# Optimization experiments

Hardware: AMD Instinct MI355X
Metric: run time of the kernel (lower is better)

## Reference

```python
import jax, jax.numpy as jnp
import numpy as np

R = 8
EPS = 1e-08
EPSS = 1e-12


def _diff_x(x, r):
    left = x[:, :, r:2 * r + 1]
    middle = x[:, :, 2 * r + 1:] - x[:, :, :-2 * r - 1]
    right = x[:, :, -1:] - x[:, :, -2 * r - 1:-r - 1]
    return jnp.concatenate([left, middle, right], axis=2)


def _diff_y(x, r):
    left = x[:, :, :, r:2 * r + 1]
    middle = x[:, :, :, 2 * r + 1:] - x[:, :, :, :-2 * r - 1]
    right = x[:, :, :, -1:] - x[:, :, :, -2 * r - 1:-r - 1]
    return jnp.concatenate([left, middle, right], axis=3)


def box_filter(x, r):
    # cumsum-based (2r+1)x(2r+1) box sum with clamped borders (matches torch BoxFilter)
    return _diff_y(jnp.cumsum(_diff_x(jnp.cumsum(x, axis=2), r), axis=3), r)


def bilinear_resize(x, H, W):
    # F.interpolate(mode='bilinear', align_corners=True) for NCHW
    n, c, h, w = x.shape
    ys = jnp.linspace(0.0, h - 1.0, H)
    xs = jnp.linspace(0.0, w - 1.0, W)
    y0 = jnp.floor(ys).astype(jnp.int32)
    x0 = jnp.floor(xs).astype(jnp.int32)
    y1 = jnp.minimum(y0 + 1, h - 1)
    x1 = jnp.minimum(x0 + 1, w - 1)
    wy = (ys - y0).astype(x.dtype)[None, None, :, None]
    wx = (xs - x0).astype(x.dtype)[None, None, None, :]
    rows = jnp.take(x, y0, axis=2) * (1.0 - wy) + jnp.take(x, y1, axis=2) * wy
    return jnp.take(rows, x0, axis=3) * (1.0 - wx) + jnp.take(rows, x1, axis=3) * wx


def setup_inputs() -> dict:
    key = jax.random.key(0)
    k1, k2, k3, k4 = jax.random.split(key, 4)
    return {
        "lr_x": jax.random.normal(k1, (4, 3, 256, 256), dtype=jnp.float32),
        "lr_y": jax.random.normal(k2, (4, 3, 256, 256), dtype=jnp.float32),
        "hr_x": jax.random.normal(k3, (4, 3, 1024, 1024), dtype=jnp.float32),
        "l_a": jax.random.uniform(k4, (4, 3, 256, 256), dtype=jnp.float32),
    }


def reference(lr_x, lr_y, hr_x, l_a):
    n, c, h, w = lr_x.shape
    _, _, hh, wh = hr_x.shape
    dt = lr_x.dtype

    N = box_filter(jnp.ones((1, 1, h, w), dtype=dt), R)  # local window counts

    l_a = jnp.abs(l_a) + EPSS
    l_t = l_a / jnp.sum(l_a)

    mean_a = box_filter(l_a) if False else box_filter(l_a, R) / N
    mean_a2xy = box_filter(l_a * l_a * lr_x * lr_y, R) / N
    mean_tax = box_filter(l_t * l_a * lr_x, R) / N
    mean_ay = box_filter(l_a * lr_y, R) / N
    mean_a2x2 = box_filter(l_a * l_a * lr_x * lr_x, R) / N
    mean_ax = box_filter(l_a * lr_x, R) / N

    temp = jnp.abs(mean_a2x2 - N * mean_tax * mean_ax)
    A = (mean_a2xy - N * mean_tax * mean_ay) / (temp + EPS)
    b = (mean_ay - A * mean_ax) / mean_a

    A = box_filter(A, R) / N
    b = box_filter(b, R) / N

    mean_A = bilinear_resize(A, hh, wh)
    mean_b = bilinear_resize(b, hh, wh)
    return (mean_A * hr_x + mean_b).astype(jnp.float32)
```

## Files before the change

### kernel.cpp

```cpp
#include <hip/hip_runtime.h>

#define RAD 8
#define HH 256
#define WW 256
#define NC 12
#define PS (HH*WW)

#define NA 52
#define NM 36
#define AP 53
#define CP 37

__device__ __forceinline__ int swz768(int b) { return (b & 7) * 96 + (b >> 3); }
__device__ __forceinline__ int swz576(int b) { return (b & 7) * 72 + (b >> 3); }

__device__ __forceinline__ float run17(float x) {
    float s = x + __shfl_up(x, 1, 64);
    s += __shfl_up(s, 2, 64);
    s += __shfl_up(s, 4, 64);
    s += __shfl_up(s, 8, 64);
    s += __shfl_up(x, 16, 64);
    return s;
}

__global__ __launch_bounds__(256) void k_reduce(const float* __restrict__ la,
                                                float* __restrict__ partials) {
    int tid = threadIdx.x;
    __shared__ float ls[4];
    const float4* p4 = (const float4*)la;
    int base = blockIdx.x * 2048 + tid;
    float s = 0.f;
    #pragma unroll
    for (int i = 0; i < 8; i++) {
        float4 v = p4[base + i * 256];
        s += (fabsf(v.x) + 1e-12f) + (fabsf(v.y) + 1e-12f) +
             (fabsf(v.z) + 1e-12f) + (fabsf(v.w) + 1e-12f);
    }
    for (int off = 32; off > 0; off >>= 1) s += __shfl_down(s, off, 64);
    int lane = tid & 63, wid = tid >> 6;
    if (lane == 0) ls[wid] = s;
    __syncthreads();
    if (tid == 0) partials[blockIdx.x] = ls[0] + ls[1] + ls[2] + ls[3];
}

__global__ __launch_bounds__(256) void k_ab(const float* __restrict__ la,
                                            const float* __restrict__ lx,
                                            const float* __restrict__ ly,
                                            const float* __restrict__ partials,
                                            float* __restrict__ Ab,
                                            float* __restrict__ Bb) {
    int tid = threadIdx.x, lane = tid & 63, wv = tid >> 6;
    int gw = swz576(blockIdx.x) * 4 + wv;
    int p  = gw / 192;
    int r  = gw - p * 192;
    int s  = r >> 5;
    int bd = r & 31;
    int i0 = bd << 3;
    int C0 = s * 48;
    int col = C0 - 8 + lane;
    bool vc = (col >= 0) && (col < WW);
    int colc = min(max(col, 0), WW - 1);
    const float* pa = la + p * PS + colc;
    const float* px = lx + p * PS + colc;
    const float* py = ly + p * PS + colc;

    float psum = partials[lane] + ((lane < 32) ? partials[lane + 64] : 0.0f);
    #pragma unroll
    for (int off = 32; off > 0; off >>= 1) psum += __shfl_xor(psum, off, 64);
    float invS = 1.0f / psum;

    int  cA  = C0 - 16 + lane;
    bool vcA = (lane >= 16) && (cA < WW);
    float cxA = (float)(min(cA + RAD, WW - 1) - max(cA - RAD, 0) + 1);

    float s0 = 0, s1 = 0, s2 = 0, s3 = 0, s4 = 0, s5 = 0;
    auto accum = [&](int rr, float sg) {
        float va = 0.f, vx = 0.f, vy = 0.f;
        if (vc) { int o = rr * WW; va = pa[o]; vx = px[o]; vy = py[o]; }
        float a  = vc ? (fabsf(va) + 1e-12f) : 0.f;
        float ax = a * vx, ay = a * vy;
        s0 = fmaf(sg, a, s0); s1 = fmaf(sg, ax, s1); s2 = fmaf(sg, ay, s2);
        s3 = fmaf(sg, a * ax, s3); s4 = fmaf(sg, ax * ax, s4); s5 = fmaf(sg, ax * ay, s5);
    };

    #pragma unroll
    for (int d = -8; d <= 8; ++d) {
        int rr = i0 + d;
        if (rr >= 0 && rr < HH) accum(rr, 1.0f);
    }

    float* Apl = Ab + p * PS;
    float* Bpl = Bb + p * PS;
    #pragma unroll
    for (int k = 0; k < 8; ++k) {
        int m = i0 + k;
        if (k > 0) {
            int ra = m + 8; if (ra < HH) accum(ra, 1.0f);
            int rs = m - 9; if (rs >= 0) accum(rs, -1.0f);
        }
        float h0 = run17(s0), h1 = run17(s1), h2 = run17(s2),
              h3 = run17(s3), h4 = run17(s4), h5 = run17(s5);
        float cy = (float)(min(m + RAD, HH - 1) - max(m - RAD, 0) + 1);
        float Nv = cxA * cy, invN = 1.0f / Nv;
        float m_a = h0 * invN, m_ax = h1 * invN, m_ay = h2 * invN;
        float m_tax = h3 * invN * invS;
        float m_a2x2 = h4 * invN, m_a2xy = h5 * invN;
        float tempv = fabsf(m_a2x2 - Nv * m_tax * m_ax);
        float Av = (m_a2xy - Nv * m_tax * m_ay) / (tempv + 1e-8f);
        float bv = (m_ay - Av * m_ax) / m_a;
        if (vcA) {
            int o = m * WW + cA;
            Apl[o] = Av;
            Bpl[o] = bv;
        }
    }
}

__global__ __launch_bounds__(256) void k_tile(const float* __restrict__ Ab,
                                              const float* __restrict__ Bb,
                                              const float* __restrict__ hrx,
                                              float* __restrict__ out) {
    __shared__ float sA[NA * AP], sB[NA * AP];
    __shared__ float sHA[NA * CP], sHB[NA * CP];
    float* mAb = sA;
    float* mBb = sB;

    int tid = threadIdx.x;
    int b  = swz768(blockIdx.x);
    int p  = b >> 6;
    int t  = b & 63;
    int ti = t >> 3, tj = t & 7;
    int I0 = ti << 7, J0 = tj << 7;
    int Lr0 = max(0, (I0 * 255) / 1023 - 1);
    int Lc0 = max(0, (J0 * 255) / 1023 - 1);

    const float* Apl = Ab + p * PS;
    const float* Bpl = Bb + p * PS;
    for (int idx = tid; idx < NA * NA; idx += 256) {
        int r = idx / NA, c = idx - r * NA;
        int gr = Lr0 - 8 + r, gc = Lc0 - 8 + c;
        float av = 0.f, bv = 0.f;
        if (gr >= 0 && gr < HH && gc >= 0 && gc < WW) {
            int o = gr * WW + gc;
            av = Apl[o]; bv = Bpl[o];
        }
        sA[r * AP + c] = av;
        sB[r * AP + c] = bv;
    }
    __syncthreads();

    for (int job = tid; job < 208; job += 256) {
        int row   = job % 52;
        int which = (job / 52) & 1;
        int strip = job / 104;
        const float* rp = (which ? sB : sA) + row * AP;
        float* dst = (which ? sHB : sHA) + row * CP;
        int c0 = strip * 18;
        float sum = 0.f;
        #pragma unroll
        for (int c = 0; c < 17; ++c) sum += rp[c0 + c];
        dst[c0] = sum;
        for (int jc = c0 + 1; jc < c0 + 18; ++jc) {
            sum += rp[jc + 16] - rp[jc - 1];
            dst[jc] = sum;
        }
    }
    __syncthreads();

    for (int job = tid; job < 144; job += 256) {
        int colc  = job % 36;
        int which = (job / 36) & 1;
        int strip = job / 72;
        const float* src = which ? sHB : sHA;
        float* dst = which ? mBb : mAb;
        int gjC = Lc0 + colc;
        float cxw = (float)(min(gjC + RAD, WW - 1) - max(gjC - RAD, 0) + 1);
        int r0 = strip * 18;
        float sum = 0.f;
        #pragma unroll
        for (int d = 0; d < 17; ++d) sum += src[(r0 + d) * CP + colc];
        for (int ic = r0; ic < r0 + 18; ++ic) {
            if (ic > r0) sum += src[(ic + 16) * CP + colc] - src[(ic - 1) * CP + colc];
            int giR = Lr0 + ic;
            float cyw = (float)(min(giR + RAD, HH - 1) - max(giR - RAD, 0) + 1);
            dst[ic * CP + colc] = sum / (cxw * cyw);
        }
    }
    __syncthreads();

    {
        int col4 = tid & 31;
        int rb   = tid >> 5;
        int J4 = (J0 >> 2) + col4;
        int Jp = J4 << 2;
        const float scale = 255.0f / 1023.0f;
        int xb = (int)((float)Jp * scale);
        int i1 = min(xb + 1, WW - 1), i2 = min(xb + 2, WW - 1);
        int lxb = xb - Lc0, li1 = i1 - Lc0, li2 = i2 - Lc0;
        float wxv[4]; bool hs[4];
        #pragma unroll
        for (int k = 0; k < 4; k++) {
            float xsk = (float)(Jp + k) * scale;
            int x0 = (int)xsk;
            wxv[k] = xsk - (float)x0;
            hs[k] = (x0 > xb);
        }
        const float4* h4 = (const float4*)hrx;
        float4* o4 = (float4*)out;
        int planeHR = p * 262144;
        #pragma unroll
        for (int it = 0; it < 16; ++it) {
            int row = (it << 3) + rb;
            int I = I0 + row;
            float ysf = (float)I * scale;
            int y0 = (int)ysf;
            float wy = ysf - (float)y0;
            int y1 = min(y0 + 1, HH - 1);
            int ly0 = y0 - Lr0, ly1 = y1 - Lr0;
            const float* a0p = mAb + ly0 * CP;
            const float* a1p = mAb + ly1 * CP;
            const float* b0p = mBb + ly0 * CP;
            const float* b1p = mBb + ly1 * CP;
            float A0a = a0p[lxb], A0b = a0p[li1], A0c = a0p[li2];
            float A1a = a1p[lxb], A1b = a1p[li1], A1c = a1p[li2];
            float B0a = b0p[lxb], B0b = b0p[li1], B0c = b0p[li2];
            float B1a = b1p[lxb], B1b = b1p[li1], B1c = b1p[li2];
            int hidx = planeHR + I * 256 + J4;
            float4 h = h4[hidx];
            float hv[4] = {h.x, h.y, h.z, h.w};
            float ov[4];
            float omwy = 1.0f - wy;
            #pragma unroll
            for (int k = 0; k < 4; k++) {
                bool hb = hs[k];
                float Alo0 = hb ? A0b : A0a, Ahi0 = hb ? A0c : A0b;
                float Alo1 = hb ? A1b : A1a, Ahi1 = hb ? A1c : A1b;
                float Blo0 = hb ? B0b : B0a, Bhi0 = hb ? B0c : B0b;
                float Blo1 = hb ? B1b : B1a, Bhi1 = hb ? B1c : B1b;
                float wx = wxv[k], omwx = 1.0f - wx;
                float Ar0 = Alo0 * omwx + Ahi0 * wx;
                float Ar1 = Alo1 * omwx + Ahi1 * wx;
                float Br0 = Blo0 * omwx + Bhi0 * wx;
                float Br1 = Blo1 * omwx + Bhi1 * wx;
                float Avv = Ar0 * omwy + Ar1 * wy;
                float Bvv = Br0 * omwy + Br1 * wy;
                ov[k] = Avv * hv[k] + Bvv;
            }
            float4 o; o.x = ov[0]; o.y = ov[1]; o.z = ov[2]; o.w = ov[3];
            o4[hidx] = o;
        }
    }
}

extern "C" void kernel_launch(void* const* d_in, const int* in_sizes, int n_in,
                              void* d_out, int out_size, void* d_ws, size_t ws_size,
                              hipStream_t stream) {
    const float* lr_x = (const float*)d_in[0];
    const float* lr_y = (const float*)d_in[1];
    const float* hr_x = (const float*)d_in[2];
    const float* l_a  = (const float*)d_in[3];
    float* out = (float*)d_out;

    float* ws       = (float*)d_ws;
    float* partials = ws;
    float* Ab       = ws + 256;
    float* Bb       = Ab + NC * PS;

    k_reduce<<<96, 256, 0, stream>>>(l_a, partials);
    k_ab    <<<576, 256, 0, stream>>>(l_a, lr_x, lr_y, partials, Ab, Bb);
    k_tile  <<<768, 256, 0, stream>>>(Ab, Bb, hr_x, out);
}
```

Before: 139.4 us.

## Shrink tiles in both kernels for more blocks and prefetch HR loads

k_ab now has each wave produce 4 output rows instead of 8, which doubles the grid to 1152 blocks. k_tile uses 64x64 output tiles instead of 128x128, giving 3072 blocks. Its smaller shared-memory box filter now sums 17 taps directly rather than using a running sum, and all four hr_x float4 loads are issued before compute. The aim is higher occupancy and latency hiding on a memory-bound pipeline, at the cost of more halo recomputation (overlapping 17-row windows and re-loaded A/B halos).

```diff
diff --git a/kernel.cpp b/kernel.cpp
--- a/kernel.cpp
+++ b/kernel.cpp
@@ -1,18 +1,20 @@
 #include <hip/hip_runtime.h>
+
 
 #define RAD 8
 #define HH 256
 #define WW 256
 #define NC 12
 #define PS (HH*WW)
-
-#define NA 52
-#define NM 36
-#define AP 53
-#define CP 37
-
-__device__ __forceinline__ int swz768(int b) { return (b & 7) * 96 + (b >> 3); }
-__device__ __forceinline__ int swz576(int b) { return (b & 7) * 72 + (b >> 3); }
+#define SCALE (255.0f/1023.0f)
+
+#define NA2 36
+#define NC2 20
+#define AP2 37
+#define HP2 21
+
+__device__ __forceinline__ int swz3072(int b) { return (b & 7) * 384 + (b >> 3); }
+__device__ __forceinline__ int swz1152(int b) { return (b & 7) * 144 + (b >> 3); }
 
 __device__ __forceinline__ float run17(float x) {
     float s = x + __shfl_up(x, 1, 64);
@@ -50,12 +52,12 @@
                                             float* __restrict__ Ab,
                                             float* __restrict__ Bb) {
     int tid = threadIdx.x, lane = tid & 63, wv = tid >> 6;
-    int gw = swz576(blockIdx.x) * 4 + wv;
-    int p  = gw / 192;
-    int r  = gw - p * 192;
-    int s  = r >> 5;
-    int bd = r & 31;
-    int i0 = bd << 3;
+    int gw = swz1152(blockIdx.x) * 4 + wv;
+    int p  = gw / 384;
+    int r  = gw - p * 384;
+    int s  = r >> 6;
+    int bd = r & 63;
+    int i0 = bd << 2;
     int C0 = s * 48;
     int col = C0 - 8 + lane;
     bool vc = (col >= 0) && (col < WW);
@@ -92,7 +94,7 @@
     float* Apl = Ab + p * PS;
     float* Bpl = Bb + p * PS;
     #pragma unroll
-    for (int k = 0; k < 8; ++k) {
+    for (int k = 0; k < 4; ++k) {
         int m = i0 + k;
         if (k > 0) {
             int ra = m + 8; if (ra < HH) accum(ra, 1.0f);
@@ -120,87 +122,74 @@
                                               const float* __restrict__ Bb,
                                               const float* __restrict__ hrx,
                                               float* __restrict__ out) {
-    __shared__ float sA[NA * AP], sB[NA * AP];
-    __shared__ float sHA[NA * CP], sHB[NA * CP];
+    __shared__ float sA[NA2 * AP2], sB[NA2 * AP2];
+    __shared__ float sHA[NA2 * HP2], sHB[NA2 * HP2];
     float* mAb = sA;
     float* mBb = sB;
 
     int tid = threadIdx.x;
-    int b  = swz768(blockIdx.x);
-    int p  = b >> 6;
-    int t  = b & 63;
-    int ti = t >> 3, tj = t & 7;
-    int I0 = ti << 7, J0 = tj << 7;
+    int b  = swz3072(blockIdx.x);
+    int p  = b >> 8;
+    int t  = b & 255;
+    int ti = t >> 4, tj = t & 15;
+    int I0 = ti << 6, J0 = tj << 6;
     int Lr0 = max(0, (I0 * 255) / 1023 - 1);
     int Lc0 = max(0, (J0 * 255) / 1023 - 1);
 
     const float* Apl = Ab + p * PS;
     const float* Bpl = Bb + p * PS;
-    for (int idx = tid; idx < NA * NA; idx += 256) {
-        int r = idx / NA, c = idx - r * NA;
+    for (int idx = tid; idx < NA2 * NA2; idx += 256) {
+        int r = idx / NA2, c = idx - r * NA2;
         int gr = Lr0 - 8 + r, gc = Lc0 - 8 + c;
         float av = 0.f, bv = 0.f;
         if (gr >= 0 && gr < HH && gc >= 0 && gc < WW) {
             int o = gr * WW + gc;
             av = Apl[o]; bv = Bpl[o];
         }
-        sA[r * AP + c] = av;
-        sB[r * AP + c] = bv;
-    }
-    __syncthreads();
-
-    for (int job = tid; job < 208; job += 256) {
-        int row   = job % 52;
-        int which = (job / 52) & 1;
-        int strip = job / 104;
-        const float* rp = (which ? sB : sA) + row * AP;
-        float* dst = (which ? sHB : sHA) + row * CP;
-        int c0 = strip * 18;
-        float sum = 0.f;
-        #pragma unroll
-        for (int c = 0; c < 17; ++c) sum += rp[c0 + c];
-        dst[c0] = sum;
-        for (int jc = c0 + 1; jc < c0 + 18; ++jc) {
-            sum += rp[jc + 16] - rp[jc - 1];
-            dst[jc] = sum;
-        }
-    }
-    __syncthreads();
-
-    for (int job = tid; job < 144; job += 256) {
-        int colc  = job % 36;
-        int which = (job / 36) & 1;
-        int strip = job / 72;
-        const float* src = which ? sHB : sHA;
-        float* dst = which ? mBb : mAb;
-        int gjC = Lc0 + colc;
-        float cxw = (float)(min(gjC + RAD, WW - 1) - max(gjC - RAD, 0) + 1);
-        int r0 = strip * 18;
-        float sum = 0.f;
-        #pragma unroll
-        for (int d = 0; d < 17; ++d) sum += src[(r0 + d) * CP + colc];
-        for (int ic = r0; ic < r0 + 18; ++ic) {
-            if (ic > r0) sum += src[(ic + 16) * CP + colc] - src[(ic - 1) * CP + colc];
-            int giR = Lr0 + ic;
-            float cyw = (float)(min(giR + RAD, HH - 1) - max(giR - RAD, 0) + 1);
-            dst[ic * CP + colc] = sum / (cxw * cyw);
-        }
+        sA[r * AP2 + c] = av;
+        sB[r * AP2 + c] = bv;
+    }
+    __syncthreads();
+
+    for (int job = tid; job < 2 * NA2 * NC2; job += 256) {
+        int which = (job >= NA2 * NC2);
+        int rest  = which ? job - NA2 * NC2 : job;
+        int r = rest / NC2, c = rest - r * NC2;
+        const float* rp = (which ? sB : sA) + r * AP2 + c;
+        float s = 0.f;
+        #pragma unroll
+        for (int j = 0; j < 17; ++j) s += rp[j];
+        (which ? sHB : sHA)[r * HP2 + c] = s;
+    }
+    __syncthreads();
+
+    for (int job = tid; job < 2 * NC2 * NC2; job += 256) {
+        int which = (job >= NC2 * NC2);
+        int rest  = which ? job - NC2 * NC2 : job;
+        int r = rest / NC2, c = rest - r * NC2;
+        const float* sp = (which ? sHB : sHA) + r * HP2 + c;
+        float s = 0.f;
+        #pragma unroll
+        for (int j = 0; j < 17; ++j) s += sp[j * HP2];
+        int gj = Lc0 + c, gi = Lr0 + r;
+        float cxw = (float)(min(gj + RAD, WW - 1) - max(gj - RAD, 0) + 1);
+        float cyw = (float)(min(gi + RAD, HH - 1) - max(gi - RAD, 0) + 1);
+        (which ? mBb : mAb)[r * HP2 + c] = s / (cxw * cyw);
     }
     __syncthreads();
 
     {
-        int col4 = tid & 31;
-        int rb   = tid >> 5;
+        int col4 = tid & 15;
+        int rg   = tid >> 4;
         int J4 = (J0 >> 2) + col4;
         int Jp = J4 << 2;
-        const float scale = 255.0f / 1023.0f;
-        int xb = (int)((float)Jp * scale);
+        int xb = (int)((float)Jp * SCALE);
         int i1 = min(xb + 1, WW - 1), i2 = min(xb + 2, WW - 1);
         int lxb = xb - Lc0, li1 = i1 - Lc0, li2 = i2 - Lc0;
         float wxv[4]; bool hs[4];
         #pragma unroll
         for (int k = 0; k < 4; k++) {
-            float xsk = (float)(Jp + k) * scale;
+            float xsk = (float)(Jp + k) * SCALE;
             int x0 = (int)xsk;
             wxv[k] = xsk - (float)x0;
             hs[k] = (x0 > xb);
@@ -208,25 +197,32 @@
         const float4* h4 = (const float4*)hrx;
         float4* o4 = (float4*)out;
         int planeHR = p * 262144;
-        #pragma unroll
-        for (int it = 0; it < 16; ++it) {
-            int row = (it << 3) + rb;
+
+        int hidx0 = planeHR + (I0 + 0 * 16 + rg) * 256 + J4;
+        int hidx1 = planeHR + (I0 + 1 * 16 + rg) * 256 + J4;
+        int hidx2 = planeHR + (I0 + 2 * 16 + rg) * 256 + J4;
+        int hidx3 = planeHR + (I0 + 3 * 16 + rg) * 256 + J4;
+        float4 hp0 = h4[hidx0], hp1 = h4[hidx1], hp2 = h4[hidx2], hp3 = h4[hidx3];
+
+        #pragma unroll
+        for (int it = 0; it < 4; ++it) {
+            int row = (it << 4) + rg;
             int I = I0 + row;
-            float ysf = (float)I * scale;
+            float ysf = (float)I * SCALE;
             int y0 = (int)ysf;
             float wy = ysf - (float)y0;
             int y1 = min(y0 + 1, HH - 1);
             int ly0 = y0 - Lr0, ly1 = y1 - Lr0;
-            const float* a0p = mAb + ly0 * CP;
-            const float* a1p = mAb + ly1 * CP;
-            const float* b0p = mBb + ly0 * CP;
-            const float* b1p = mBb + ly1 * CP;
+            const float* a0p = mAb + ly0 * HP2;
+            const float* a1p = mAb + ly1 * HP2;
+            const float* b0p = mBb + ly0 * HP2;
+            const float* b1p = mBb + ly1 * HP2;
             float A0a = a0p[lxb], A0b = a0p[li1], A0c = a0p[li2];
             float A1a = a1p[lxb], A1b = a1p[li1], A1c = a1p[li2];
             float B0a = b0p[lxb], B0b = b0p[li1], B0c = b0p[li2];
             float B1a = b1p[lxb], B1b = b1p[li1], B1c = b1p[li2];
-            int hidx = planeHR + I * 256 + J4;
-            float4 h = h4[hidx];
+            float4 h = (it == 0) ? hp0 : (it == 1) ? hp1 : (it == 2) ? hp2 : hp3;
+            int hidx = (it == 0) ? hidx0 : (it == 1) ? hidx1 : (it == 2) ? hidx2 : hidx3;
             float hv[4] = {h.x, h.y, h.z, h.w};
             float ov[4];
             float omwy = 1.0f - wy;
@@ -267,6 +263,6 @@
     float* Bb       = Ab + NC * PS;
 
     k_reduce<<<96, 256, 0, stream>>>(l_a, partials);
-    k_ab    <<<576, 256, 0, stream>>>(l_a, lr_x, lr_y, partials, Ab, Bb);
-    k_tile  <<<768, 256, 0, stream>>>(Ab, Bb, hr_x, out);
-}
+    k_ab    <<<1152, 256, 0, stream>>>(l_a, lr_x, lr_y, partials, Ab, Bb);
+    k_tile  <<<3072, 256, 0, stream>>>(Ab, Bb, hr_x, out);
+}
```

After: 138.1 us. Within noise of the previous version (-0.9%).
